# Optimization experiments

Hardware: AMD Instinct MI355X
Metric: run time of the kernel (lower is better)

## Reference

```python
import jax, jax.numpy as jnp
import numpy as np

DIM = 4096
N_HEADS = 32
N_KV_HEADS = 8
HEAD_DIM = 128
EPS = 1e-6
SEQ = 2048
N_SEG = 4
SEG_LEN = SEQ // N_SEG


def setup_inputs() -> dict:
    key = jax.random.key(0)
    ks = jax.random.split(key, 6)
    s = 0.02
    x = jax.random.normal(ks[0], (1, SEQ, DIM), jnp.float32)
    wq = jax.random.normal(ks[1], (N_HEADS * HEAD_DIM, DIM), jnp.float32) * s
    wk = jax.random.normal(ks[2], (N_KV_HEADS * HEAD_DIM, DIM), jnp.float32) * s
    wv = jax.random.normal(ks[3], (N_KV_HEADS * HEAD_DIM, DIM), jnp.float32) * s
    wo = jax.random.normal(ks[4], (DIM, N_HEADS * HEAD_DIM), jnp.float32) * s
    q_norm_w = jnp.ones((HEAD_DIM,), jnp.float32)
    k_norm_w = jnp.ones((HEAD_DIM,), jnp.float32)
    # RoPE cache: [max_pos, head_dim//2, 2] = (cos, sin)
    inv_freq = 1.0 / (10000.0 ** (jnp.arange(0, HEAD_DIM // 2, dtype=jnp.float32) / (HEAD_DIM // 2)))
    t = jnp.arange(SEQ, dtype=jnp.float32)
    freqs = jnp.outer(t, inv_freq)  # [SEQ, hd/2]
    rope_cache = jnp.stack([jnp.cos(freqs), jnp.sin(freqs)], axis=-1)
    # packed varlen: 4 segments of 512, positions restart per segment
    positions = (jnp.arange(SEQ, dtype=jnp.int32) % SEG_LEN)[None, :]
    cu_seqlens = jnp.arange(N_SEG + 1, dtype=jnp.int32) * SEG_LEN
    return {"x": x, "wq": wq, "wk": wk, "wv": wv, "wo": wo,
            "q_norm_w": q_norm_w, "k_norm_w": k_norm_w,
            "rope_cache": rope_cache, "positions": positions,
            "cu_seqlens": cu_seqlens}


def _rms_norm(x, w):
    xf = x.astype(jnp.float32)
    var = jnp.mean(xf * xf, axis=-1, keepdims=True)
    return w * (xf * jax.lax.rsqrt(var + EPS))


def _apply_rope(x, rope_cache, positions):
    # x: [bs, S, h, hd]; rope_cache: [P, hd/2, 2]; positions: [bs, S]
    cs = rope_cache[positions]                    # [bs, S, hd/2, 2]
    cos = cs[..., 0][:, :, None, :]               # [bs, S, 1, hd/2]
    sin = cs[..., 1][:, :, None, :]
    half = x.shape[-1] // 2
    x1, x2 = x[..., :half], x[..., half:]
    return jnp.concatenate([x1 * cos - x2 * sin, x2 * cos + x1 * sin], axis=-1)


def reference(x, wq, wk, wv, wo, q_norm_w, k_norm_w, rope_cache, positions, cu_seqlens):
    bs, S, _ = x.shape
    n_rep = N_HEADS // N_KV_HEADS
    xq = (x @ wq.T).reshape(bs, S, N_HEADS, HEAD_DIM)
    xk = (x @ wk.T).reshape(bs, S, N_KV_HEADS, HEAD_DIM)
    xv = (x @ wv.T).reshape(bs, S, N_KV_HEADS, HEAD_DIM)
    xq = _rms_norm(xq, q_norm_w)
    xk = _rms_norm(xk, k_norm_w)
    xq = _apply_rope(xq, rope_cache, positions)
    xk = _apply_rope(xk, rope_cache, positions)
    # GQA: repeat kv heads
    xk = jnp.repeat(xk, n_rep, axis=2)
    xv = jnp.repeat(xv, n_rep, axis=2)
    q = xq.transpose(0, 2, 1, 3)  # [bs, h, S, hd]
    k = xk.transpose(0, 2, 1, 3)
    v = xv.transpose(0, 2, 1, 3)
    # varlen mask: causal within each packed segment
    idx = jnp.arange(S)
    seg = jnp.searchsorted(cu_seqlens, idx, side='right') - 1  # [S]
    mask = (seg[:, None] == seg[None, :]) & (idx[:, None] >= idx[None, :])
    scale = HEAD_DIM ** -0.5
    scores = jnp.einsum('bhqd,bhkd->bhqk', q, k) * scale
    scores = jnp.where(mask[None, None], scores, jnp.float32(-1e30))
    probs = jax.nn.softmax(scores, axis=-1)
    out = jnp.einsum('bhqk,bhkd->bhqd', probs, v)
    out = out.transpose(0, 2, 1, 3).reshape(bs, S, N_HEADS * HEAD_DIM)
    return out @ wo.T
```

## Files before the change

kernel.cpp:

```cpp
#include <hip/hip_runtime.h>

typedef __bf16 bf16_t;
typedef __bf16 bf16x8 __attribute__((ext_vector_type(8)));
typedef __bf16 bf16x4 __attribute__((ext_vector_type(4)));
typedef float f32x4 __attribute__((ext_vector_type(4)));

#define SEQL 2048
#define DIMM 4096
#define NH 32
#define NKV 8
#define HD 128

__device__ __forceinline__ void gl2lds16(const void* g, void* l) {
  __builtin_amdgcn_global_load_lds((__attribute__((address_space(1))) void*)g,
                                   (__attribute__((address_space(3))) void*)l,
                                   16, 0, 0);
}

__global__ __launch_bounds__(256) void cvt5_kernel(const float* __restrict__ s0,
                                                   const float* __restrict__ s1,
                                                   const float* __restrict__ s2,
                                                   const float* __restrict__ s3,
                                                   const float* __restrict__ s4,
                                                   bf16_t* __restrict__ dst) {
  const long base = (long)blockIdx.x * 4096;
  const float* s;
  long o;
  if (base < 8388608L)       { s = s0; o = base; }
  else if (base < 25165824L) { s = s1; o = base - 8388608L; }
  else if (base < 29360128L) { s = s2; o = base - 25165824L; }
  else if (base < 33554432L) { s = s3; o = base - 29360128L; }
  else                       { s = s4; o = base - 33554432L; }
  const long t4 = threadIdx.x * 4;
#pragma unroll
  for (int j = 0; j < 4; ++j) {
    const long e = t4 + j * 1024;
    float4 v = *(const float4*)(s + o + e);
    bf16x4 ov;
    ov[0] = (bf16_t)v.x; ov[1] = (bf16_t)v.y; ov[2] = (bf16_t)v.z; ov[3] = (bf16_t)v.w;
    *(bf16x4*)(dst + base + e) = ov;
  }
}

#define TS 136
#define QSCALE (0.08838834764831845f * 1.4426950408889634f)
__global__ __launch_bounds__(256, 3) void gemm_qkv_kernel(const bf16_t* __restrict__ A,
                                                          const bf16_t* __restrict__ B,
                                                          const float* __restrict__ qnw,
                                                          const float* __restrict__ knw,
                                                          const float* __restrict__ rope,
                                                          const int* __restrict__ pos,
                                                          bf16_t* __restrict__ Qb,
                                                          bf16_t* __restrict__ Kb,
                                                          bf16_t* __restrict__ Vb) {
  __shared__ __align__(16) bf16_t smem[128 * TS];
  bf16_t* lA = smem;
  bf16_t* lB = smem + 8192;
  const int K = DIMM, npanel = 6;
  const int tid = threadIdx.x;
  const int lin = blockIdx.x;
  const int xcd = lin & 7, idx = lin >> 3;
  const int bm = (idx & 15) * 128;
  const int bn = ((idx >> 4) + xcd * npanel) * 128;
  const int lane = tid & 63, wave = tid >> 6;
  const int wm = (wave >> 1) * 64, wn = (wave & 1) * 64;
  const int lr = lane & 15, quad = lane >> 4;

  f32x4 acc[4][4];
#pragma unroll
  for (int mi = 0; mi < 4; ++mi)
#pragma unroll
    for (int ni = 0; ni < 4; ++ni)
      acc[mi][ni] = (f32x4){0.f, 0.f, 0.f, 0.f};

  long soff[4];
#pragma unroll
  for (int c = 0; c < 4; ++c) {
    const int s = tid + 256 * c;
    soff[c] = (long)(s >> 3) * K + (((s & 7) ^ ((s >> 3) & 7)) << 3);
  }
  const bf16_t* Abase = A + (long)bm * K;
  const bf16_t* Bbase = B + (long)bn * K;

  for (int k0 = 0; k0 < K; k0 += 64) {
    __syncthreads();
#pragma unroll
    for (int c = 0; c < 4; ++c) {
      gl2lds16(Abase + soff[c] + k0, lA + (tid + 256 * c) * 8);
      gl2lds16(Bbase + soff[c] + k0, lB + (tid + 256 * c) * 8);
    }
    __syncthreads();
#pragma unroll
    for (int ks = 0; ks < 2; ++ks) {
      bf16x8 af[4], bfr[4];
#pragma unroll
      for (int mi = 0; mi < 4; ++mi)
        af[mi] = *(const bf16x8*)&lA[(wm + mi * 16 + lr) * 64 + ((((ks << 2) | quad) ^ (lr & 7)) << 3)];
#pragma unroll
      for (int ni = 0; ni < 4; ++ni)
        bfr[ni] = *(const bf16x8*)&lB[(wn + ni * 16 + lr) * 64 + ((((ks << 2) | quad) ^ (lr & 7)) << 3)];
#pragma unroll
      for (int mi = 0; mi < 4; ++mi)
#pragma unroll
        for (int ni = 0; ni < 4; ++ni)
          acc[mi][ni] = __builtin_amdgcn_mfma_f32_16x16x32_bf16(af[mi], bfr[ni], acc[mi][ni], 0, 0, 0);
    }
  }

  __syncthreads();
  bf16_t* tile = smem;
#pragma unroll
  for (int mi = 0; mi < 4; ++mi)
#pragma unroll
    for (int ni = 0; ni < 4; ++ni)
#pragma unroll
      for (int r = 0; r < 4; ++r)
        tile[(wm + mi * 16 + quad * 4 + r) * TS + wn + ni * 16 + lr] = (bf16_t)acc[mi][ni][r];
  __syncthreads();

  if (bn < 5120) {
    const bool isQ = bn < 4096;
    const float* nwp = isQ ? qnw : knw;
    const float osc = isQ ? QSCALE : 1.0f;
    bf16_t* outp = isQ ? (Qb + (long)(bn >> 7) * SEQL * HD)
                       : (Kb + (long)((bn - 4096) >> 7) * SEQL * HD);
    const int r = tid >> 1, hf = tid & 1;
    bf16x8 rowv[16];
#pragma unroll
    for (int j = 0; j < 16; ++j) rowv[j] = *(const bf16x8*)&tile[r * TS + j * 8];
    float ss = 0.f;
#pragma unroll
    for (int j = 0; j < 16; ++j)
#pragma unroll
      for (int e = 0; e < 8; ++e) { const float f = (float)rowv[j][e]; ss += f * f; }
    const float sc = rsqrtf(ss * (1.0f / 128.0f) + 1e-6f) * osc;
    const int p = pos[bm + r];
    const float* rp = rope + p * 128;
    bf16_t obuf[64];
#pragma unroll
    for (int g = 0; g < 8; ++g) {
#pragma unroll
      for (int e = 0; e < 8; ++e) {
        const int i = g * 8 + e;
        const float2 cs = *(const float2*)(rp + 2 * i);
        const float nlo = (float)rowv[i >> 3][i & 7] * sc * nwp[i];
        const float nhi = (float)rowv[8 + (i >> 3)][i & 7] * sc * nwp[64 + i];
        obuf[i] = (bf16_t)(hf ? (nhi * cs.x + nlo * cs.y) : (nlo * cs.x - nhi * cs.y));
      }
    }
    bf16_t* op = outp + (long)(bm + r) * HD + hf * 64;
#pragma unroll
    for (int g = 0; g < 8; ++g) *(bf16x8*)(op + g * 8) = *(const bf16x8*)&obuf[g * 8];
  } else {
    const int hk = (bn - 5120) >> 7;
    const int d = tid & 127, shalf = tid >> 7;
    bf16_t* vp = Vb + ((long)hk * HD + d) * SEQL + bm + shalf * 64;
#pragma unroll
    for (int grp = 0; grp < 8; ++grp) {
      bf16x8 t;
#pragma unroll
      for (int e = 0; e < 8; ++e) t[e] = tile[(shalf * 64 + grp * 8 + e) * TS + d];
      *(bf16x8*)(vp + grp * 8) = t;
    }
  }
}

template <typename CT>
__global__ __launch_bounds__(256, 3) void gemm_bt_kernel(const bf16_t* __restrict__ A,
                                                         const bf16_t* __restrict__ B,
                                                         CT* __restrict__ C,
                                                         int N, int K, int npanel) {
  __shared__ bf16_t lA[128 * 64];
  __shared__ bf16_t lB[128 * 64];
  const int tid = threadIdx.x;
  const int lin = blockIdx.x;
  const int xcd = lin & 7, idx = lin >> 3;
  const int bm = (idx & 15) * 128;
  const int bn = ((idx >> 4) + xcd * npanel) * 128;
  const int lane = tid & 63, wave = tid >> 6;
  const int wm = (wave >> 1) * 64, wn = (wave & 1) * 64;
  const int lr = lane & 15, quad = lane >> 4;

  f32x4 acc[4][4];
#pragma unroll
  for (int mi = 0; mi < 4; ++mi)
#pragma unroll
    for (int ni = 0; ni < 4; ++ni)
      acc[mi][ni] = (f32x4){0.f, 0.f, 0.f, 0.f};

  long soff[4];
#pragma unroll
  for (int c = 0; c < 4; ++c) {
    const int s = tid + 256 * c;
    soff[c] = (long)(s >> 3) * K + (((s & 7) ^ ((s >> 3) & 7)) << 3);
  }
  const bf16_t* Abase = A + (long)bm * K;
  const bf16_t* Bbase = B + (long)bn * K;

  for (int k0 = 0; k0 < K; k0 += 64) {
    __syncthreads();
#pragma unroll
    for (int c = 0; c < 4; ++c) {
      gl2lds16(Abase + soff[c] + k0, lA + (tid + 256 * c) * 8);
      gl2lds16(Bbase + soff[c] + k0, lB + (tid + 256 * c) * 8);
    }
    __syncthreads();
#pragma unroll
    for (int ks = 0; ks < 2; ++ks) {
      bf16x8 af[4], bfr[4];
#pragma unroll
      for (int mi = 0; mi < 4; ++mi)
        af[mi] = *(const bf16x8*)&lA[(wm + mi * 16 + lr) * 64 + ((((ks << 2) | quad) ^ (lr & 7)) << 3)];
#pragma unroll
      for (int ni = 0; ni < 4; ++ni)
        bfr[ni] = *(const bf16x8*)&lB[(wn + ni * 16 + lr) * 64 + ((((ks << 2) | quad) ^ (lr & 7)) << 3)];
#pragma unroll
      for (int mi = 0; mi < 4; ++mi)
#pragma unroll
        for (int ni = 0; ni < 4; ++ni)
          acc[mi][ni] = __builtin_amdgcn_mfma_f32_16x16x32_bf16(af[mi], bfr[ni], acc[mi][ni], 0, 0, 0);
    }
  }

#pragma unroll
  for (int mi = 0; mi < 4; ++mi) {
    const int row = bm + wm + mi * 16 + quad * 4;
#pragma unroll
    for (int ni = 0; ni < 4; ++ni) {
      const int col = bn + wn + ni * 16 + lr;
      CT* cp = C + (long)row * N + col;
#pragma unroll
      for (int r = 0; r < 4; ++r) cp[(long)r * N] = (CT)acc[mi][ni][r];
    }
  }
}

#define CK 64
#define PSTR 72
__global__ __launch_bounds__(256) void attn_kernel(const bf16_t* __restrict__ Q,
                                                   const bf16_t* __restrict__ Kt,
                                                   const bf16_t* __restrict__ Vt,
                                                   bf16_t* __restrict__ O) {
  __shared__ bf16_t lK[CK * 128];
  __shared__ bf16_t lV[144 * CK];
  __shared__ bf16_t lP[128 * PSTR];
  const int lin = blockIdx.x;
  const int qb = (lin < 256) ? (3 - (lin & 1)) : (lin & 1);
  const int gh = (lin >> 1) & 127;
  const int h = gh & 31, g = gh >> 5;
  const int hk = h >> 2;
  const int tid = threadIdx.x, lane = tid & 63, wave = tid >> 6;
  const int lr = lane & 15, quad = lane >> 4;
  const int s_base = g * 512 + qb * 128;

  if (tid < 128) {
    bf16x8 one8;
#pragma unroll
    for (int j = 0; j < 8; ++j) one8[j] = (bf16_t)1.0f;
    *(bf16x8*)&lV[128 * CK + tid * 8] = one8;
  }

  bf16x8 qf[2][4];
  const bf16_t* Qp = Q + ((long)h * SEQL + s_base + wave * 32 + lr) * HD + quad * 8;
#pragma unroll
  for (int mi = 0; mi < 2; ++mi)
#pragma unroll
    for (int ks = 0; ks < 4; ++ks)
      qf[mi][ks] = *(const bf16x8*)(Qp + mi * 16 * HD + ks * 32);

  f32x4 oacc[2][9];
#pragma unroll
  for (int mi = 0; mi < 2; ++mi)
#pragma unroll
    for (int di = 0; di < 9; ++di) oacc[mi][di] = (f32x4){0.f, 0.f, 0.f, 0.f};

  const int nchunk = 2 * qb + 2;
  for (int c = 0; c < nchunk; ++c) {
    __syncthreads();
    {
      const bf16_t* Kg = Kt + ((long)hk * SEQL + g * 512 + c * CK) * HD;
      const bf16_t* Vg = Vt + (long)hk * HD * SEQL + g * 512 + c * CK;
#pragma unroll
      for (int cc = 0; cc < 4; ++cc) {
        const int i = tid + 256 * cc;
        gl2lds16(Kg + (long)(i >> 4) * HD + (i & 15) * 8, lK + i * 8);
        gl2lds16(Vg + (long)(i >> 3) * SEQL + (i & 7) * 8, lV + i * 8);
      }
    }
    __syncthreads();

    f32x4 sv[2][4];
#pragma unroll
    for (int mi = 0; mi < 2; ++mi)
#pragma unroll
      for (int ni = 0; ni < 4; ++ni) sv[mi][ni] = (f32x4){0.f, 0.f, 0.f, 0.f};
#pragma unroll
    for (int ks = 0; ks < 4; ++ks) {
#pragma unroll
      for (int ni = 0; ni < 4; ++ni) {
        const bf16x8 kf = *(const bf16x8*)&lK[(ni * 16 + lr) * 128 + ks * 32 + quad * 8];
        sv[0][ni] = __builtin_amdgcn_mfma_f32_16x16x32_bf16(qf[0][ks], kf, sv[0][ni], 0, 0, 0);
        sv[1][ni] = __builtin_amdgcn_mfma_f32_16x16x32_bf16(qf[1][ks], kf, sv[1][ni], 0, 0, 0);
      }
    }

#pragma unroll
    for (int mi = 0; mi < 2; ++mi)
#pragma unroll
      for (int ni = 0; ni < 4; ++ni)
#pragma unroll
        for (int r = 0; r < 4; ++r) {
          const int colseg = c * CK + ni * 16 + lr;
          const int rowseg = qb * 128 + wave * 32 + mi * 16 + quad * 4 + r;
          float p = exp2f(sv[mi][ni][r]);
          p = (colseg > rowseg) ? 0.f : p;
          lP[(wave * 32 + mi * 16 + quad * 4 + r) * PSTR + ni * 16 + lr] = (bf16_t)p;
        }
    __syncthreads();

#pragma unroll
    for (int ks = 0; ks < 2; ++ks) {
      const bf16x8 pf0 = *(const bf16x8*)&lP[(wave * 32 + lr) * PSTR + ks * 32 + quad * 8];
      const bf16x8 pf1 = *(const bf16x8*)&lP[(wave * 32 + 16 + lr) * PSTR + ks * 32 + quad * 8];
#pragma unroll
      for (int di = 0; di < 9; ++di) {
        const bf16x8 vfr = *(const bf16x8*)&lV[(di * 16 + lr) * CK + ks * 32 + quad * 8];
        oacc[0][di] = __builtin_amdgcn_mfma_f32_16x16x32_bf16(pf0, vfr, oacc[0][di], 0, 0, 0);
        oacc[1][di] = __builtin_amdgcn_mfma_f32_16x16x32_bf16(pf1, vfr, oacc[1][di], 0, 0, 0);
      }
    }
  }

#pragma unroll
  for (int mi = 0; mi < 2; ++mi)
#pragma unroll
    for (int r = 0; r < 4; ++r) {
      const float inv = 1.0f / oacc[mi][8][r];
      const int row = s_base + wave * 32 + mi * 16 + quad * 4 + r;
      bf16_t* opp = O + (long)row * DIMM + h * HD + lr;
#pragma unroll
      for (int di = 0; di < 8; ++di) opp[di * 16] = (bf16_t)(oacc[mi][di][r] * inv);
    }
}

extern "C" void kernel_launch(void* const* d_in, const int* in_sizes, int n_in,
                              void* d_out, int out_size, void* d_ws, size_t ws_size,
                              hipStream_t stream) {
  (void)in_sizes; (void)n_in; (void)out_size; (void)ws_size;
  const float* x    = (const float*)d_in[0];
  const float* wq   = (const float*)d_in[1];
  const float* wk   = (const float*)d_in[2];
  const float* wv   = (const float*)d_in[3];
  const float* wo   = (const float*)d_in[4];
  const float* qnw  = (const float*)d_in[5];
  const float* knw  = (const float*)d_in[6];
  const float* rope = (const float*)d_in[7];
  const int*   pos  = (const int*)d_in[8];
  float* out = (float*)d_out;

  char* ws = (char*)d_ws;
  size_t off = 0;
  auto alloc = [&](size_t b) { char* p = ws + off; off += (b + 255) & ~(size_t)255; return p; };
  bf16_t* xb    = (bf16_t*)alloc((size_t)SEQL * DIMM * 2);
  bf16_t* wqkvb = (bf16_t*)alloc((size_t)DIMM * DIMM * 2);
  alloc((size_t)NKV * HD * DIMM * 2);
  alloc((size_t)NKV * HD * DIMM * 2);
  bf16_t* wob   = (bf16_t*)alloc((size_t)DIMM * DIMM * 2);
  bf16_t* Qb    = (bf16_t*)alloc((size_t)NH * SEQL * HD * 2);
  bf16_t* Kb    = (bf16_t*)alloc((size_t)NKV * SEQL * HD * 2);
  bf16_t* Vb    = (bf16_t*)alloc((size_t)NKV * SEQL * HD * 2);
  bf16_t* attnb = xb;

  cvt5_kernel<<<dim3(12288), 256, 0, stream>>>(x, wq, wk, wv, wo, xb);
  gemm_qkv_kernel<<<dim3(768), 256, 0, stream>>>(xb, wqkvb, qnw, knw, rope, pos, Qb, Kb, Vb);
  attn_kernel<<<dim3(512), 256, 0, stream>>>(Qb, Kb, Vb, attnb);
  gemm_bt_kernel<float><<<dim3(512), 256, 0, stream>>>(attnb, wob, out, DIMM, DIMM, 4);
}
```

Baseline: 432.0 us.

## Rewrite QKV GEMM with 256x256 tiles and 4-stage async LDS pipeline

Replaces the 128x128 QKV projection GEMM with a 512-thread 256x256-tile kernel. It uses a 4-slot LDS ring with BK=32, prefetches two stages ahead through global_load_lds, and interleaves barriers and setprio around the MFMA blocks. The goal is to hide global load latency and raise operand reuse per tile. The norm/RoPE and V-transpose epilogue is split into two 128-row halves so it fits in the 128 KB shared buffer. The trade-off is only 192 blocks, which underfills 256 CUs, plus much higher register and LDS pressure.

```diff
diff --git a/kernel.cpp b/kernel.cpp
--- a/kernel.cpp
+++ b/kernel.cpp
@@ -42,125 +42,164 @@
   }
 }
 
-#define TS 136
+#define BK2 32
+#define EPS 264
 #define QSCALE (0.08838834764831845f * 1.4426950408889634f)
-__global__ __launch_bounds__(256, 3) void gemm_qkv_kernel(const bf16_t* __restrict__ A,
-                                                          const bf16_t* __restrict__ B,
-                                                          const float* __restrict__ qnw,
-                                                          const float* __restrict__ knw,
-                                                          const float* __restrict__ rope,
-                                                          const int* __restrict__ pos,
-                                                          bf16_t* __restrict__ Qb,
-                                                          bf16_t* __restrict__ Kb,
-                                                          bf16_t* __restrict__ Vb) {
-  __shared__ __align__(16) bf16_t smem[128 * TS];
-  bf16_t* lA = smem;
-  bf16_t* lB = smem + 8192;
-  const int K = DIMM, npanel = 6;
+__global__ __launch_bounds__(512, 2) void gemm_qkv8(const bf16_t* __restrict__ A,
+                                                    const bf16_t* __restrict__ B,
+                                                    const float* __restrict__ qnw,
+                                                    const float* __restrict__ knw,
+                                                    const float* __restrict__ rope,
+                                                    const int* __restrict__ pos,
+                                                    bf16_t* __restrict__ Qb,
+                                                    bf16_t* __restrict__ Kb,
+                                                    bf16_t* __restrict__ Vb) {
+  __shared__ __align__(16) bf16_t smem[65536];
+  const int K = DIMM;
+  const int NT = K / BK2;
   const int tid = threadIdx.x;
   const int lin = blockIdx.x;
   const int xcd = lin & 7, idx = lin >> 3;
-  const int bm = (idx & 15) * 128;
-  const int bn = ((idx >> 4) + xcd * npanel) * 128;
+  const int bm = (idx & 7) * 256;
+  const int bn = ((idx >> 3) + xcd * 3) * 256;
   const int lane = tid & 63, wave = tid >> 6;
-  const int wm = (wave >> 1) * 64, wn = (wave & 1) * 64;
+  const int wrow = wave >> 2, wcol = wave & 3;
+  const int wm = wrow * 128, wn = wcol * 64;
   const int lr = lane & 15, quad = lane >> 4;
-
-  f32x4 acc[4][4];
-#pragma unroll
-  for (int mi = 0; mi < 4; ++mi)
+  const int swz = (quad ^ ((lr >> 1) & 3)) << 3;
+
+  long asrc[2]; int adst[2];
+#pragma unroll
+  for (int c = 0; c < 2; ++c) {
+    const int id = tid + 512 * c;
+    asrc[c] = (long)(id >> 2) * K + (long)((((id & 3) ^ ((id >> 3) & 3)) << 3));
+    adst[c] = id * 8;
+  }
+  const bf16_t* Abase = A + (long)bm * K;
+  const bf16_t* Bbase = B + (long)bn * K;
+
+  f32x4 acc[8][4];
+#pragma unroll
+  for (int mi = 0; mi < 8; ++mi)
 #pragma unroll
     for (int ni = 0; ni < 4; ++ni)
       acc[mi][ni] = (f32x4){0.f, 0.f, 0.f, 0.f};
 
-  long soff[4];
-#pragma unroll
-  for (int c = 0; c < 4; ++c) {
-    const int s = tid + 256 * c;
-    soff[c] = (long)(s >> 3) * K + (((s & 7) ^ ((s >> 3) & 7)) << 3);
-  }
-  const bf16_t* Abase = A + (long)bm * K;
-  const bf16_t* Bbase = B + (long)bn * K;
-
-  for (int k0 = 0; k0 < K; k0 += 64) {
-    __syncthreads();
-#pragma unroll
-    for (int c = 0; c < 4; ++c) {
-      gl2lds16(Abase + soff[c] + k0, lA + (tid + 256 * c) * 8);
-      gl2lds16(Bbase + soff[c] + k0, lB + (tid + 256 * c) * 8);
-    }
-    __syncthreads();
-#pragma unroll
-    for (int ks = 0; ks < 2; ++ks) {
-      bf16x8 af[4], bfr[4];
-#pragma unroll
-      for (int mi = 0; mi < 4; ++mi)
-        af[mi] = *(const bf16x8*)&lA[(wm + mi * 16 + lr) * 64 + ((((ks << 2) | quad) ^ (lr & 7)) << 3)];
+#define STAGE(t, c)                                                              \
+  do {                                                                           \
+    const int slot_ = (t) & 3;                                                   \
+    const long k0_ = (long)(t) * BK2;                                            \
+    gl2lds16(Abase + asrc[c] + k0_, smem + slot_ * 8192 + adst[c]);              \
+    gl2lds16(Bbase + asrc[c] + k0_, smem + 32768 + slot_ * 8192 + adst[c]);      \
+  } while (0)
+
+  STAGE(0, 0); STAGE(0, 1); STAGE(1, 0); STAGE(1, 1);
+  asm volatile("s_waitcnt vmcnt(4)" ::: "memory");
+  __builtin_amdgcn_s_barrier();
+
+  for (int t = 0; t < NT; ++t) {
+    const bf16_t* As = smem + (t & 3) * 8192;
+    const bf16_t* Bs = smem + 32768 + (t & 3) * 8192;
+    bf16x8 af[4], bfr[4];
+#pragma unroll
+    for (int mi = 0; mi < 4; ++mi)
+      af[mi] = *(const bf16x8*)&As[(wm + mi * 16 + lr) * 32 + swz];
+#pragma unroll
+    for (int ni = 0; ni < 4; ++ni)
+      bfr[ni] = *(const bf16x8*)&Bs[(wn + ni * 16 + lr) * 32 + swz];
+    if (t + 2 < NT) STAGE(t + 2, 0);
+    __builtin_amdgcn_s_barrier();
+    asm volatile("s_waitcnt lgkmcnt(0)" ::: "memory");
+    __builtin_amdgcn_sched_barrier(0);
+    __builtin_amdgcn_s_setprio(1);
+#pragma unroll
+    for (int mi = 0; mi < 4; ++mi)
 #pragma unroll
       for (int ni = 0; ni < 4; ++ni)
-        bfr[ni] = *(const bf16x8*)&lB[(wn + ni * 16 + lr) * 64 + ((((ks << 2) | quad) ^ (lr & 7)) << 3)];
-#pragma unroll
-      for (int mi = 0; mi < 4; ++mi)
+        acc[mi][ni] = __builtin_amdgcn_mfma_f32_16x16x32_bf16(af[mi], bfr[ni], acc[mi][ni], 0, 0, 0);
+    __builtin_amdgcn_s_setprio(0);
+    __builtin_amdgcn_s_barrier();
+#pragma unroll
+    for (int mi = 0; mi < 4; ++mi)
+      af[mi] = *(const bf16x8*)&As[(wm + 64 + mi * 16 + lr) * 32 + swz];
+    if (t + 2 < NT) STAGE(t + 2, 1);
+    __builtin_amdgcn_s_barrier();
+    asm volatile("s_waitcnt lgkmcnt(0)" ::: "memory");
+    __builtin_amdgcn_sched_barrier(0);
+    __builtin_amdgcn_s_setprio(1);
+#pragma unroll
+    for (int mi = 0; mi < 4; ++mi)
+#pragma unroll
+      for (int ni = 0; ni < 4; ++ni)
+        acc[4 + mi][ni] = __builtin_amdgcn_mfma_f32_16x16x32_bf16(af[mi], bfr[ni], acc[4 + mi][ni], 0, 0, 0);
+    __builtin_amdgcn_s_setprio(0);
+    if (t + 2 < NT) { asm volatile("s_waitcnt vmcnt(4)" ::: "memory"); }
+    else            { asm volatile("s_waitcnt vmcnt(0)" ::: "memory"); }
+    __builtin_amdgcn_s_barrier();
+  }
+#undef STAGE
+
+  const bool isQ = bn < 4096;
+  const bool isV = bn >= 5120;
+#pragma unroll 1
+  for (int half = 0; half < 2; ++half) {
+    __syncthreads();
+    if (wrow == half) {
+#pragma unroll
+      for (int mi = 0; mi < 8; ++mi)
 #pragma unroll
         for (int ni = 0; ni < 4; ++ni)
-          acc[mi][ni] = __builtin_amdgcn_mfma_f32_16x16x32_bf16(af[mi], bfr[ni], acc[mi][ni], 0, 0, 0);
-    }
-  }
-
-  __syncthreads();
-  bf16_t* tile = smem;
-#pragma unroll
-  for (int mi = 0; mi < 4; ++mi)
-#pragma unroll
-    for (int ni = 0; ni < 4; ++ni)
-#pragma unroll
-      for (int r = 0; r < 4; ++r)
-        tile[(wm + mi * 16 + quad * 4 + r) * TS + wn + ni * 16 + lr] = (bf16_t)acc[mi][ni][r];
-  __syncthreads();
-
-  if (bn < 5120) {
-    const bool isQ = bn < 4096;
-    const float* nwp = isQ ? qnw : knw;
-    const float osc = isQ ? QSCALE : 1.0f;
-    bf16_t* outp = isQ ? (Qb + (long)(bn >> 7) * SEQL * HD)
-                       : (Kb + (long)((bn - 4096) >> 7) * SEQL * HD);
-    const int r = tid >> 1, hf = tid & 1;
-    bf16x8 rowv[16];
-#pragma unroll
-    for (int j = 0; j < 16; ++j) rowv[j] = *(const bf16x8*)&tile[r * TS + j * 8];
-    float ss = 0.f;
-#pragma unroll
-    for (int j = 0; j < 16; ++j)
-#pragma unroll
-      for (int e = 0; e < 8; ++e) { const float f = (float)rowv[j][e]; ss += f * f; }
-    const float sc = rsqrtf(ss * (1.0f / 128.0f) + 1e-6f) * osc;
-    const int p = pos[bm + r];
-    const float* rp = rope + p * 128;
-    bf16_t obuf[64];
-#pragma unroll
-    for (int g = 0; g < 8; ++g) {
-#pragma unroll
-      for (int e = 0; e < 8; ++e) {
-        const int i = g * 8 + e;
-        const float2 cs = *(const float2*)(rp + 2 * i);
-        const float nlo = (float)rowv[i >> 3][i & 7] * sc * nwp[i];
-        const float nhi = (float)rowv[8 + (i >> 3)][i & 7] * sc * nwp[64 + i];
-        obuf[i] = (bf16_t)(hf ? (nhi * cs.x + nlo * cs.y) : (nlo * cs.x - nhi * cs.y));
+#pragma unroll
+          for (int r = 0; r < 4; ++r)
+            smem[(mi * 16 + quad * 4 + r) * EPS + wn + ni * 16 + lr] = (bf16_t)acc[mi][ni][r];
+    }
+    __syncthreads();
+    const int growb = bm + half * 128;
+    if (!isV) {
+      const int r = tid >> 2, hh = (tid >> 1) & 1, hf = tid & 1;
+      const int cb = bn + hh * 128;
+      const float* nwp = isQ ? qnw : knw;
+      const float osc = isQ ? QSCALE : 1.0f;
+      bf16_t* outp = isQ ? (Qb + (long)(cb >> 7) * SEQL * HD)
+                         : (Kb + (long)((cb - 4096) >> 7) * SEQL * HD);
+      bf16x8 rowv[16];
+#pragma unroll
+      for (int j = 0; j < 16; ++j) rowv[j] = *(const bf16x8*)&smem[r * EPS + hh * 128 + j * 8];
+      float ss = 0.f;
+#pragma unroll
+      for (int j = 0; j < 16; ++j)
+#pragma unroll
+        for (int e = 0; e < 8; ++e) { const float f = (float)rowv[j][e]; ss += f * f; }
+      const float sc = rsqrtf(ss * (1.0f / 128.0f) + 1e-6f) * osc;
+      const int p = pos[growb + r];
+      const float* rp = rope + p * 128;
+      bf16_t obuf[64];
+#pragma unroll
+      for (int g = 0; g < 8; ++g) {
+#pragma unroll
+        for (int e = 0; e < 8; ++e) {
+          const int i = g * 8 + e;
+          const float2 cs = *(const float2*)(rp + 2 * i);
+          const float nlo = (float)rowv[i >> 3][i & 7] * sc * nwp[i];
+          const float nhi = (float)rowv[8 + (i >> 3)][i & 7] * sc * nwp[64 + i];
+          obuf[i] = (bf16_t)(hf ? (nhi * cs.x + nlo * cs.y) : (nlo * cs.x - nhi * cs.y));
+        }
       }
-    }
-    bf16_t* op = outp + (long)(bm + r) * HD + hf * 64;
-#pragma unroll
-    for (int g = 0; g < 8; ++g) *(bf16x8*)(op + g * 8) = *(const bf16x8*)&obuf[g * 8];
-  } else {
-    const int hk = (bn - 5120) >> 7;
-    const int d = tid & 127, shalf = tid >> 7;
-    bf16_t* vp = Vb + ((long)hk * HD + d) * SEQL + bm + shalf * 64;
-#pragma unroll
-    for (int grp = 0; grp < 8; ++grp) {
-      bf16x8 t;
-#pragma unroll
-      for (int e = 0; e < 8; ++e) t[e] = tile[(shalf * 64 + grp * 8 + e) * TS + d];
-      *(bf16x8*)(vp + grp * 8) = t;
+      bf16_t* op = outp + (long)(growb + r) * HD + hf * 64;
+#pragma unroll
+      for (int g = 0; g < 8; ++g) *(bf16x8*)(op + g * 8) = *(const bf16x8*)&obuf[g * 8];
+    } else {
+      const int d = tid & 127, q2 = tid >> 7;
+      const int hh = q2 >> 1, shalf = q2 & 1;
+      const int hv = ((bn - 5120) >> 7) + hh;
+      bf16_t* vp = Vb + ((long)hv * HD + d) * SEQL + growb + shalf * 64;
+#pragma unroll
+      for (int grp = 0; grp < 8; ++grp) {
+        bf16x8 tv;
+#pragma unroll
+        for (int e = 0; e < 8; ++e) tv[e] = smem[(shalf * 64 + grp * 8 + e) * EPS + hh * 128 + d];
+        *(bf16x8*)(vp + grp * 8) = tv;
+      }
     }
   }
 }
@@ -372,7 +411,7 @@
   bf16_t* attnb = xb;
 
   cvt5_kernel<<<dim3(12288), 256, 0, stream>>>(x, wq, wk, wv, wo, xb);
-  gemm_qkv_kernel<<<dim3(768), 256, 0, stream>>>(xb, wqkvb, qnw, knw, rope, pos, Qb, Kb, Vb);
+  gemm_qkv8<<<dim3(192), 512, 0, stream>>>(xb, wqkvb, qnw, knw, rope, pos, Qb, Kb, Vb);
   attn_kernel<<<dim3(512), 256, 0, stream>>>(Qb, Kb, Vb, attnb);
   gemm_bt_kernel<float><<<dim3(512), 256, 0, stream>>>(attnb, wob, out, DIMM, DIMM, 4);
 }
```

New measurement: 531.1 us. 23.0% more time.

## Triple-buffer GEMM K-loop with async global-to-LDS prefetch two stages ahead

Applied to the files above, without the earlier changes.

Both the QKV GEMM and the generic GEMM replace the single-buffered 64-wide K loop, which synchronised twice per step, with a three-slot ring of 32-wide K tiles in LDS. Each slot is loaded by global_load_lds two iterations ahead, with explicit vmcnt waits and raw s_barrier, so global latency overlaps with MFMA work. It also raises wave priority around the MFMA block and uses a new swizzle for the 32-wide rows. The trade-offs are more LDS per block (48KB), which may limit occupancy at launch bounds of 3, and hand-written waitcnt logic that is fragile.

```diff
diff --git a/kernel.cpp b/kernel.cpp
--- a/kernel.cpp
+++ b/kernel.cpp
@@ -53,10 +53,146 @@
                                                           bf16_t* __restrict__ Qb,
                                                           bf16_t* __restrict__ Kb,
                                                           bf16_t* __restrict__ Vb) {
-  __shared__ __align__(16) bf16_t smem[128 * TS];
-  bf16_t* lA = smem;
-  bf16_t* lB = smem + 8192;
-  const int K = DIMM, npanel = 6;
+  __shared__ __align__(16) bf16_t smem[24576];
+  const int K = DIMM;
+  const int NT = K / 32;
+  const int tid = threadIdx.x;
+  const int lin = blockIdx.x;
+  const int xcd = lin & 7, idx = lin >> 3;
+  const int bm = (idx & 15) * 128;
+  const int bn = ((idx >> 4) + xcd * 6) * 128;
+  const int lane = tid & 63, wave = tid >> 6;
+  const int wm = (wave >> 1) * 64, wn = (wave & 1) * 64;
+  const int lr = lane & 15, quad = lane >> 4;
+  const int swz = (quad ^ ((lr >> 1) & 3)) << 3;
+
+  long src0, src1;
+  int dst0, dst1;
+  {
+    const int id0 = tid, id1 = tid + 256;
+    src0 = (long)(id0 >> 2) * K + (((id0 & 3) ^ ((id0 >> 3) & 3)) << 3);
+    src1 = (long)(id1 >> 2) * K + (((id1 & 3) ^ ((id1 >> 3) & 3)) << 3);
+    dst0 = id0 * 8;
+    dst1 = id1 * 8;
+  }
+  const bf16_t* Abase = A + (long)bm * K;
+  const bf16_t* Bbase = B + (long)bn * K;
+
+  f32x4 acc[4][4];
+#pragma unroll
+  for (int mi = 0; mi < 4; ++mi)
+#pragma unroll
+    for (int ni = 0; ni < 4; ++ni)
+      acc[mi][ni] = (f32x4){0.f, 0.f, 0.f, 0.f};
+
+#define STG(sl_, t_)                                                  \
+  do {                                                                \
+    const long k0_ = (long)(t_) * 32;                                 \
+    gl2lds16(Abase + src0 + k0_, smem + (sl_) * 4096 + dst0);         \
+    gl2lds16(Abase + src1 + k0_, smem + (sl_) * 4096 + dst1);         \
+    gl2lds16(Bbase + src0 + k0_, smem + 12288 + (sl_) * 4096 + dst0); \
+    gl2lds16(Bbase + src1 + k0_, smem + 12288 + (sl_) * 4096 + dst1); \
+  } while (0)
+
+  STG(0, 0); STG(1, 1);
+  asm volatile("s_waitcnt vmcnt(4)" ::: "memory");
+  __builtin_amdgcn_s_barrier();
+
+  int rs = 0, ss = 2;
+  for (int t = 0; t < NT; ++t) {
+    const bf16_t* As = smem + rs * 4096;
+    const bf16_t* Bs = smem + 12288 + rs * 4096;
+    bf16x8 af[4], bfr[4];
+#pragma unroll
+    for (int mi = 0; mi < 4; ++mi)
+      af[mi] = *(const bf16x8*)&As[(wm + mi * 16 + lr) * 32 + swz];
+#pragma unroll
+    for (int ni = 0; ni < 4; ++ni)
+      bfr[ni] = *(const bf16x8*)&Bs[(wn + ni * 16 + lr) * 32 + swz];
+    if (t + 2 < NT) STG(ss, t + 2);
+    __builtin_amdgcn_s_barrier();
+    asm volatile("s_waitcnt lgkmcnt(0)" ::: "memory");
+    __builtin_amdgcn_sched_barrier(0);
+    __builtin_amdgcn_s_setprio(1);
+#pragma unroll
+    for (int mi = 0; mi < 4; ++mi)
+#pragma unroll
+      for (int ni = 0; ni < 4; ++ni)
+        acc[mi][ni] = __builtin_amdgcn_mfma_f32_16x16x32_bf16(af[mi], bfr[ni], acc[mi][ni], 0, 0, 0);
+    __builtin_amdgcn_s_setprio(0);
+    if (t + 2 < NT) { asm volatile("s_waitcnt vmcnt(4)" ::: "memory"); }
+    else            { asm volatile("s_waitcnt vmcnt(0)" ::: "memory"); }
+    __builtin_amdgcn_s_barrier();
+    rs = (rs == 2) ? 0 : rs + 1;
+    ss = (ss == 2) ? 0 : ss + 1;
+  }
+#undef STG
+
+  __syncthreads();
+  bf16_t* tile = smem;
+#pragma unroll
+  for (int mi = 0; mi < 4; ++mi)
+#pragma unroll
+    for (int ni = 0; ni < 4; ++ni)
+#pragma unroll
+      for (int r = 0; r < 4; ++r)
+        tile[(wm + mi * 16 + quad * 4 + r) * TS + wn + ni * 16 + lr] = (bf16_t)acc[mi][ni][r];
+  __syncthreads();
+
+  if (bn < 5120) {
+    const bool isQ = bn < 4096;
+    const float* nwp = isQ ? qnw : knw;
+    const float osc = isQ ? QSCALE : 1.0f;
+    bf16_t* outp = isQ ? (Qb + (long)(bn >> 7) * SEQL * HD)
+                       : (Kb + (long)((bn - 4096) >> 7) * SEQL * HD);
+    const int r = tid >> 1, hf = tid & 1;
+    bf16x8 rowv[16];
+#pragma unroll
+    for (int j = 0; j < 16; ++j) rowv[j] = *(const bf16x8*)&tile[r * TS + j * 8];
+    float ss2 = 0.f;
+#pragma unroll
+    for (int j = 0; j < 16; ++j)
+#pragma unroll
+      for (int e = 0; e < 8; ++e) { const float f = (float)rowv[j][e]; ss2 += f * f; }
+    const float sc = rsqrtf(ss2 * (1.0f / 128.0f) + 1e-6f) * osc;
+    const int p = pos[bm + r];
+    const float* rp = rope + p * 128;
+    bf16_t obuf[64];
+#pragma unroll
+    for (int g = 0; g < 8; ++g) {
+#pragma unroll
+      for (int e = 0; e < 8; ++e) {
+        const int i = g * 8 + e;
+        const float2 cs = *(const float2*)(rp + 2 * i);
+        const float nlo = (float)rowv[i >> 3][i & 7] * sc * nwp[i];
+        const float nhi = (float)rowv[8 + (i >> 3)][i & 7] * sc * nwp[64 + i];
+        obuf[i] = (bf16_t)(hf ? (nhi * cs.x + nlo * cs.y) : (nlo * cs.x - nhi * cs.y));
+      }
+    }
+    bf16_t* op = outp + (long)(bm + r) * HD + hf * 64;
+#pragma unroll
+    for (int g = 0; g < 8; ++g) *(bf16x8*)(op + g * 8) = *(const bf16x8*)&obuf[g * 8];
+  } else {
+    const int hk = (bn - 5120) >> 7;
+    const int d = tid & 127, shalf = tid >> 7;
+    bf16_t* vp = Vb + ((long)hk * HD + d) * SEQL + bm + shalf * 64;
+#pragma unroll
+    for (int grp = 0; grp < 8; ++grp) {
+      bf16x8 tv;
+#pragma unroll
+      for (int e = 0; e < 8; ++e) tv[e] = tile[(shalf * 64 + grp * 8 + e) * TS + d];
+      *(bf16x8*)(vp + grp * 8) = tv;
+    }
+  }
+}
+
+template <typename CT>
+__global__ __launch_bounds__(256, 3) void gemm_bt_kernel(const bf16_t* __restrict__ A,
+                                                         const bf16_t* __restrict__ B,
+                                                         CT* __restrict__ C,
+                                                         int N, int K, int npanel) {
+  __shared__ __align__(16) bf16_t smem[24576];
+  const int NT = K >> 5;
   const int tid = threadIdx.x;
   const int lin = blockIdx.x;
   const int xcd = lin & 7, idx = lin >> 3;
@@ -65,6 +201,19 @@
   const int lane = tid & 63, wave = tid >> 6;
   const int wm = (wave >> 1) * 64, wn = (wave & 1) * 64;
   const int lr = lane & 15, quad = lane >> 4;
+  const int swz = (quad ^ ((lr >> 1) & 3)) << 3;
+
+  long src0, src1;
+  int dst0, dst1;
+  {
+    const int id0 = tid, id1 = tid + 256;
+    src0 = (long)(id0 >> 2) * K + (((id0 & 3) ^ ((id0 >> 3) & 3)) << 3);
+    src1 = (long)(id1 >> 2) * K + (((id1 & 3) ^ ((id1 >> 3) & 3)) << 3);
+    dst0 = id0 * 8;
+    dst1 = id1 * 8;
+  }
+  const bf16_t* Abase = A + (long)bm * K;
+  const bf16_t* Bbase = B + (long)bn * K;
 
   f32x4 acc[4][4];
 #pragma unroll
@@ -73,154 +222,48 @@
     for (int ni = 0; ni < 4; ++ni)
       acc[mi][ni] = (f32x4){0.f, 0.f, 0.f, 0.f};
 
-  long soff[4];
-#pragma unroll
-  for (int c = 0; c < 4; ++c) {
-    const int s = tid + 256 * c;
-    soff[c] = (long)(s >> 3) * K + (((s & 7) ^ ((s >> 3) & 7)) << 3);
-  }
-  const bf16_t* Abase = A + (long)bm * K;
-  const bf16_t* Bbase = B + (long)bn * K;
-
-  for (int k0 = 0; k0 < K; k0 += 64) {
-    __syncthreads();
-#pragma unroll
-    for (int c = 0; c < 4; ++c) {
-      gl2lds16(Abase + soff[c] + k0, lA + (tid + 256 * c) * 8);
-      gl2lds16(Bbase + soff[c] + k0, lB + (tid + 256 * c) * 8);
-    }
-    __syncthreads();
-#pragma unroll
-    for (int ks = 0; ks < 2; ++ks) {
-      bf16x8 af[4], bfr[4];
-#pragma unroll
-      for (int mi = 0; mi < 4; ++mi)
-        af[mi] = *(const bf16x8*)&lA[(wm + mi * 16 + lr) * 64 + ((((ks << 2) | quad) ^ (lr & 7)) << 3)];
+#define STG(sl_, t_)                                                  \
+  do {                                                                \
+    const long k0_ = (long)(t_) * 32;                                 \
+    gl2lds16(Abase + src0 + k0_, smem + (sl_) * 4096 + dst0);         \
+    gl2lds16(Abase + src1 + k0_, smem + (sl_) * 4096 + dst1);         \
+    gl2lds16(Bbase + src0 + k0_, smem + 12288 + (sl_) * 4096 + dst0); \
+    gl2lds16(Bbase + src1 + k0_, smem + 12288 + (sl_) * 4096 + dst1); \
+  } while (0)
+
+  STG(0, 0); STG(1, 1);
+  asm volatile("s_waitcnt vmcnt(4)" ::: "memory");
+  __builtin_amdgcn_s_barrier();
+
+  int rs = 0, ss = 2;
+  for (int t = 0; t < NT; ++t) {
+    const bf16_t* As = smem + rs * 4096;
+    const bf16_t* Bs = smem + 12288 + rs * 4096;
+    bf16x8 af[4], bfr[4];
+#pragma unroll
+    for (int mi = 0; mi < 4; ++mi)
+      af[mi] = *(const bf16x8*)&As[(wm + mi * 16 + lr) * 32 + swz];
+#pragma unroll
+    for (int ni = 0; ni < 4; ++ni)
+      bfr[ni] = *(const bf16x8*)&Bs[(wn + ni * 16 + lr) * 32 + swz];
+    if (t + 2 < NT) STG(ss, t + 2);
+    __builtin_amdgcn_s_barrier();
+    asm volatile("s_waitcnt lgkmcnt(0)" ::: "memory");
+    __builtin_amdgcn_sched_barrier(0);
+    __builtin_amdgcn_s_setprio(1);
+#pragma unroll
+    for (int mi = 0; mi < 4; ++mi)
 #pragma unroll
       for (int ni = 0; ni < 4; ++ni)
-        bfr[ni] = *(const bf16x8*)&lB[(wn + ni * 16 + lr) * 64 + ((((ks << 2) | quad) ^ (lr & 7)) << 3)];
-#pragma unroll
-      for (int mi = 0; mi < 4; ++mi)
-#pragma unroll
-        for (int ni = 0; ni < 4; ++ni)
-          acc[mi][ni] = __builtin_amdgcn_mfma_f32_16x16x32_bf16(af[mi], bfr[ni], acc[mi][ni], 0, 0, 0);
-    }
-  }
-
-  __syncthreads();
-  bf16_t* tile = smem;
-#pragma unroll
-  for (int mi = 0; mi < 4; ++mi)
-#pragma unroll
-    for (int ni = 0; ni < 4; ++ni)
-#pragma unroll
-      for (int r = 0; r < 4; ++r)
-        tile[(wm + mi * 16 + quad * 4 + r) * TS + wn + ni * 16 + lr] = (bf16_t)acc[mi][ni][r];
-  __syncthreads();
-
-  if (bn < 5120) {
-    const bool isQ = bn < 4096;
-    const float* nwp = isQ ? qnw : knw;
-    const float osc = isQ ? QSCALE : 1.0f;
-    bf16_t* outp = isQ ? (Qb + (long)(bn >> 7) * SEQL * HD)
-                       : (Kb + (long)((bn - 4096) >> 7) * SEQL * HD);
-    const int r = tid >> 1, hf = tid & 1;
-    bf16x8 rowv[16];
-#pragma unroll
-    for (int j = 0; j < 16; ++j) rowv[j] = *(const bf16x8*)&tile[r * TS + j * 8];
-    float ss = 0.f;
-#pragma unroll
-    for (int j = 0; j < 16; ++j)
-#pragma unroll
-      for (int e = 0; e < 8; ++e) { const float f = (float)rowv[j][e]; ss += f * f; }
-    const float sc = rsqrtf(ss * (1.0f / 128.0f) + 1e-6f) * osc;
-    const int p = pos[bm + r];
-    const float* rp = rope + p * 128;
-    bf16_t obuf[64];
-#pragma unroll
-    for (int g = 0; g < 8; ++g) {
-#pragma unroll
-      for (int e = 0; e < 8; ++e) {
-        const int i = g * 8 + e;
-        const float2 cs = *(const float2*)(rp + 2 * i);
-        const float nlo = (float)rowv[i >> 3][i & 7] * sc * nwp[i];
-        const float nhi = (float)rowv[8 + (i >> 3)][i & 7] * sc * nwp[64 + i];
-        obuf[i] = (bf16_t)(hf ? (nhi * cs.x + nlo * cs.y) : (nlo * cs.x - nhi * cs.y));
-      }
-    }
-    bf16_t* op = outp + (long)(bm + r) * HD + hf * 64;
-#pragma unroll
-    for (int g = 0; g < 8; ++g) *(bf16x8*)(op + g * 8) = *(const bf16x8*)&obuf[g * 8];
-  } else {
-    const int hk = (bn - 5120) >> 7;
-    const int d = tid & 127, shalf = tid >> 7;
-    bf16_t* vp = Vb + ((long)hk * HD + d) * SEQL + bm + shalf * 64;
-#pragma unroll
-    for (int grp = 0; grp < 8; ++grp) {
-      bf16x8 t;
-#pragma unroll
-      for (int e = 0; e < 8; ++e) t[e] = tile[(shalf * 64 + grp * 8 + e) * TS + d];
-      *(bf16x8*)(vp + grp * 8) = t;
-    }
-  }
-}
-
-template <typename CT>
-__global__ __launch_bounds__(256, 3) void gemm_bt_kernel(const bf16_t* __restrict__ A,
-                                                         const bf16_t* __restrict__ B,
-                                                         CT* __restrict__ C,
-                                                         int N, int K, int npanel) {
-  __shared__ bf16_t lA[128 * 64];
-  __shared__ bf16_t lB[128 * 64];
-  const int tid = threadIdx.x;
-  const int lin = blockIdx.x;
-  const int xcd = lin & 7, idx = lin >> 3;
-  const int bm = (idx & 15) * 128;
-  const int bn = ((idx >> 4) + xcd * npanel) * 128;
-  const int lane = tid & 63, wave = tid >> 6;
-  const int wm = (wave >> 1) * 64, wn = (wave & 1) * 64;
-  const int lr = lane & 15, quad = lane >> 4;
-
-  f32x4 acc[4][4];
-#pragma unroll
-  for (int mi = 0; mi < 4; ++mi)
-#pragma unroll
-    for (int ni = 0; ni < 4; ++ni)
-      acc[mi][ni] = (f32x4){0.f, 0.f, 0.f, 0.f};
-
-  long soff[4];
-#pragma unroll
-  for (int c = 0; c < 4; ++c) {
-    const int s = tid + 256 * c;
-    soff[c] = (long)(s >> 3) * K + (((s & 7) ^ ((s >> 3) & 7)) << 3);
-  }
-  const bf16_t* Abase = A + (long)bm * K;
-  const bf16_t* Bbase = B + (long)bn * K;
-
-  for (int k0 = 0; k0 < K; k0 += 64) {
-    __syncthreads();
-#pragma unroll
-    for (int c = 0; c < 4; ++c) {
-      gl2lds16(Abase + soff[c] + k0, lA + (tid + 256 * c) * 8);
-      gl2lds16(Bbase + soff[c] + k0, lB + (tid + 256 * c) * 8);
-    }
-    __syncthreads();
-#pragma unroll
-    for (int ks = 0; ks < 2; ++ks) {
-      bf16x8 af[4], bfr[4];
-#pragma unroll
-      for (int mi = 0; mi < 4; ++mi)
-        af[mi] = *(const bf16x8*)&lA[(wm + mi * 16 + lr) * 64 + ((((ks << 2) | quad) ^ (lr & 7)) << 3)];
-#pragma unroll
-      for (int ni = 0; ni < 4; ++ni)
-        bfr[ni] = *(const bf16x8*)&lB[(wn + ni * 16 + lr) * 64 + ((((ks << 2) | quad) ^ (lr & 7)) << 3)];
-#pragma unroll
-      for (int mi = 0; mi < 4; ++mi)
-#pragma unroll
-        for (int ni = 0; ni < 4; ++ni)
-          acc[mi][ni] = __builtin_amdgcn_mfma_f32_16x16x32_bf16(af[mi], bfr[ni], acc[mi][ni], 0, 0, 0);
-    }
-  }
+        acc[mi][ni] = __builtin_amdgcn_mfma_f32_16x16x32_bf16(af[mi], bfr[ni], acc[mi][ni], 0, 0, 0);
+    __builtin_amdgcn_s_setprio(0);
+    if (t + 2 < NT) { asm volatile("s_waitcnt vmcnt(4)" ::: "memory"); }
+    else            { asm volatile("s_waitcnt vmcnt(0)" ::: "memory"); }
+    __builtin_amdgcn_s_barrier();
+    rs = (rs == 2) ? 0 : rs + 1;
+    ss = (ss == 2) ? 0 : ss + 1;
+  }
+#undef STG
 
 #pragma unroll
   for (int mi = 0; mi < 4; ++mi) {
```

Measured after the change: 462.3 us. 7.0% more time.

## Double-buffer K tiles and overlap V loads with QK^T in attention kernel

Applied to the files above, without the earlier changes.

The attention kernel now double-buffers K in LDS, prefetching the next chunk's K while computing the current one. V for the current chunk is issued at the top of the iteration and waited on with fine-grained vmcnt counts only before the PV MFMAs, so its latency hides behind QK^T and the softmax. It also raises wave priority around MFMA blocks. This doubles K's LDS footprint, which may reduce occupancy, and depends on the hand-counted vmcnt waits being correct.

```diff
diff --git a/kernel.cpp b/kernel.cpp
--- a/kernel.cpp
+++ b/kernel.cpp
@@ -241,7 +241,7 @@
                                                    const bf16_t* __restrict__ Kt,
                                                    const bf16_t* __restrict__ Vt,
                                                    bf16_t* __restrict__ O) {
-  __shared__ bf16_t lK[CK * 128];
+  __shared__ bf16_t lK[2 * CK * 128];
   __shared__ bf16_t lV[144 * CK];
   __shared__ bf16_t lP[128 * PSTR];
   const int lin = blockIdx.x;
@@ -274,35 +274,58 @@
 #pragma unroll
     for (int di = 0; di < 9; ++di) oacc[mi][di] = (f32x4){0.f, 0.f, 0.f, 0.f};
 
+  const bf16_t* Kg0 = Kt + ((long)hk * SEQL + g * 512) * HD;
+  const bf16_t* Vg0 = Vt + (long)hk * HD * SEQL + g * 512;
+
+#define STGK(c_, buf_)                                                        \
+  do {                                                                        \
+    const bf16_t* Kg = Kg0 + (long)(c_) * CK * HD;                            \
+    _Pragma("unroll")                                                         \
+    for (int cc = 0; cc < 4; ++cc) {                                          \
+      const int i = tid + 256 * cc;                                           \
+      gl2lds16(Kg + (long)(i >> 4) * HD + (i & 15) * 8,                       \
+               lK + (buf_) * (CK * 128) + i * 8);                             \
+    }                                                                         \
+  } while (0)
+#define STGV(c_)                                                              \
+  do {                                                                        \
+    const bf16_t* Vg = Vg0 + (long)(c_) * CK;                                 \
+    _Pragma("unroll")                                                         \
+    for (int cc = 0; cc < 4; ++cc) {                                          \
+      const int i = tid + 256 * cc;                                           \
+      gl2lds16(Vg + (long)(i >> 3) * SEQL + (i & 7) * 8, lV + i * 8);         \
+    }                                                                         \
+  } while (0)
+
   const int nchunk = 2 * qb + 2;
+  STGK(0, 0);
+  STGV(0);
+
   for (int c = 0; c < nchunk; ++c) {
     __syncthreads();
-    {
-      const bf16_t* Kg = Kt + ((long)hk * SEQL + g * 512 + c * CK) * HD;
-      const bf16_t* Vg = Vt + (long)hk * HD * SEQL + g * 512 + c * CK;
-#pragma unroll
-      for (int cc = 0; cc < 4; ++cc) {
-        const int i = tid + 256 * cc;
-        gl2lds16(Kg + (long)(i >> 4) * HD + (i & 15) * 8, lK + i * 8);
-        gl2lds16(Vg + (long)(i >> 3) * SEQL + (i & 7) * 8, lV + i * 8);
-      }
-    }
-    __syncthreads();
-
+    if (c > 0) STGV(c);
+    if (c + 1 < nchunk) STGK(c + 1, (c + 1) & 1);
+    if (c + 1 < nchunk) { asm volatile("s_waitcnt vmcnt(8)" ::: "memory"); }
+    else                { asm volatile("s_waitcnt vmcnt(4)" ::: "memory"); }
+    __syncthreads();
+
+    const bf16_t* lKc = lK + (c & 1) * (CK * 128);
     f32x4 sv[2][4];
 #pragma unroll
     for (int mi = 0; mi < 2; ++mi)
 #pragma unroll
       for (int ni = 0; ni < 4; ++ni) sv[mi][ni] = (f32x4){0.f, 0.f, 0.f, 0.f};
+    __builtin_amdgcn_s_setprio(1);
 #pragma unroll
     for (int ks = 0; ks < 4; ++ks) {
 #pragma unroll
       for (int ni = 0; ni < 4; ++ni) {
-        const bf16x8 kf = *(const bf16x8*)&lK[(ni * 16 + lr) * 128 + ks * 32 + quad * 8];
+        const bf16x8 kf = *(const bf16x8*)&lKc[(ni * 16 + lr) * 128 + ks * 32 + quad * 8];
         sv[0][ni] = __builtin_amdgcn_mfma_f32_16x16x32_bf16(qf[0][ks], kf, sv[0][ni], 0, 0, 0);
         sv[1][ni] = __builtin_amdgcn_mfma_f32_16x16x32_bf16(qf[1][ks], kf, sv[1][ni], 0, 0, 0);
       }
     }
+    __builtin_amdgcn_s_setprio(0);
 
 #pragma unroll
     for (int mi = 0; mi < 2; ++mi)
@@ -316,8 +339,11 @@
           p = (colseg > rowseg) ? 0.f : p;
           lP[(wave * 32 + mi * 16 + quad * 4 + r) * PSTR + ni * 16 + lr] = (bf16_t)p;
         }
-    __syncthreads();
-
+    if (c + 1 < nchunk) { asm volatile("s_waitcnt vmcnt(4)" ::: "memory"); }
+    else                { asm volatile("s_waitcnt vmcnt(0)" ::: "memory"); }
+    __syncthreads();
+
+    __builtin_amdgcn_s_setprio(1);
 #pragma unroll
     for (int ks = 0; ks < 2; ++ks) {
       const bf16x8 pf0 = *(const bf16x8*)&lP[(wave * 32 + lr) * PSTR + ks * 32 + quad * 8];
@@ -329,7 +355,10 @@
         oacc[1][di] = __builtin_amdgcn_mfma_f32_16x16x32_bf16(pf1, vfr, oacc[1][di], 0, 0, 0);
       }
     }
-  }
+    __builtin_amdgcn_s_setprio(0);
+  }
+#undef STGK
+#undef STGV
 
 #pragma unroll
   for (int mi = 0; mi < 2; ++mi)
```

Measured after the change: 425.4 us. About the same (-1.5%).
